# Kernel optimization log

Measured on AMD Instinct MI355X. Metric: run time of the kernel, lower is better.

## Reference

```python
import jax, jax.numpy as jnp
import numpy as np

# decoded layout constants
NN, NO, SD = 16, 8, 4          # num_neighbors, num_obstacles, state_dim_per_agent
B = 131072                      # batch rows
H1, E, HP, AD = 64, 16, 64, 2   # phi hidden, embed, psi hidden, action dim
D_ROBOT, D_OBST = 0.3, 0.3
B_GAMMA, B_EXPH = 0.05, 1.0
PHI_MIN, PHI_MAX = -2.0, 2.0
A_MAX = 2.0


def setup_inputs() -> dict:
    key = jax.random.key(0)
    kx, kw = jax.random.split(key)
    # x: [count | goal(SD) | NN neighbor rel-states (SD each) | NO obstacle rel-pos (2 each)]
    x = jax.random.normal(kx, (B, 1 + SD + SD * NN + 2 * NO), dtype=jnp.float32) * 2.0
    x = x.at[:, 0].set(float(NN))
    names = [("Wp1n", (SD, H1)), ("bp1n", (H1,)), ("Wp2n", (H1, E)), ("bp2n", (E,)),
             ("Wr1n", (E, H1)), ("br1n", (H1,)), ("Wr2n", (H1, E)), ("br2n", (E,)),
             ("Wp1o", (2, H1)), ("bp1o", (H1,)), ("Wp2o", (H1, E)), ("bp2o", (E,)),
             ("Wr1o", (E, H1)), ("br1o", (H1,)), ("Wr2o", (H1, E)), ("br2o", (E,)),
             ("Wpsi1", (2 * E + SD, HP)), ("bpsi1", (HP,)), ("Wpsi2", (HP, AD)), ("bpsi2", (AD,))]
    ks = jax.random.split(kw, len(names))
    inp = {"x": x}
    for (n, sh), k in zip(names, ks):
        s = 1.0 / np.sqrt(sh[0])  # torch Linear default init scale
        inp[n] = jax.random.uniform(k, sh, jnp.float32, -s, s)
    return inp


def _mlp2(h, W1, b1, W2, b2):
    # Feedforward: activation between layers, linear output
    return jax.nn.relu(h @ W1 + b1) @ W2 + b2


def _deepset(el, Wp1, bp1, Wp2, bp2, Wr1, br1, Wr2, br2):
    # el: [B, n, d] -> phi each element, sum over set, rho
    phi = _mlp2(el, Wp1, bp1, Wp2, bp2)          # [B, n, E]
    return _mlp2(phi.sum(axis=1), Wr1, br1, Wr2, br2)  # [B, E]


def _barrier_sum(P, D):
    # P: [B, n, 2]; APF barrier gamma * P / (|P| * (|P|-D)^exph), summed over n
    nrm = jnp.linalg.norm(P, axis=-1, keepdims=True)   # [B, n, 1]
    H = nrm - D
    return (B_GAMMA * P / (nrm * H ** B_EXPH)).sum(axis=1)  # [B, 2]


def reference(x, Wp1n, bp1n, Wp2n, bp2n, Wr1n, br1n, Wr2n, br2n,
              Wp1o, bp1o, Wp2o, bp2o, Wr1o, br1o, Wr2o, br2o,
              Wpsi1, bpsi1, Wpsi2, bpsi2):
    nb = x.shape[0]
    g = x[:, 1:1 + SD]                                        # goal
    nbr = x[:, 1 + SD:1 + SD + SD * NN].reshape(nb, NN, SD)   # neighbor rel-states
    obs = x[:, 1 + SD + SD * NN:].reshape(nb, NO, 2)          # obstacle rel-pos

    rho_n = _deepset(nbr, Wp1n, bp1n, Wp2n, bp2n, Wr1n, br1n, Wr2n, br2n)
    rho_o = _deepset(obs, Wp1o, bp1o, Wp2o, bp2o, Wr1o, br1o, Wr2o, br2o)

    h = jnp.concatenate([rho_n, rho_o, g], axis=1)            # [B, 2E+SD]
    emp = _mlp2(h, Wpsi1, bpsi1, Wpsi2, bpsi2)                # psi network
    emp = (jnp.tanh(emp) + 1.0) / 2.0 * (PHI_MAX - PHI_MIN) + PHI_MIN  # scale_empty

    bar = _barrier_sum(-nbr[:, :, :2], D_ROBOT) + _barrier_sum(-obs, D_OBST)

    action = emp + bar
    # scale(): divide rows whose inf-norm exceeds a_max
    inv_alpha = jnp.maximum(jnp.max(jnp.abs(action), axis=1, keepdims=True) / A_MAX, 1.0)
    return action / inv_alpha
```

## Files before the change

### kernel.cpp

```cpp
#include <hip/hip_runtime.h>
#include <math.h>


typedef __attribute__((ext_vector_type(8))) _Float16 f16x8;
typedef __attribute__((ext_vector_type(2))) __fp16 fp16x2;
typedef __attribute__((ext_vector_type(4))) float f32x4;

#define XW 85

#define FR_S1N  0
#define FR_S1O  4
#define FR_G2N  8
#define FR_G2O  10
#define FR_RNA  12
#define FR_RNB  16
#define FR_ROA  18
#define FR_ROB  22
#define FR_PSI1 24
#define FR_PSI2 32
#define N_FRAGS 34

#define BIG_STR 144
#define PHI_STR 80
#define CAT_STR 144
#define L_BIG  0
#define L_PHI  2304
#define L_CAT  3584
#define L_OUT  5888
#define L_BAR  6016
#define L_OBA  6144
#define GRP_LDS 6688
#define NBA_STR 136
#define OBA_STR 68

#define H16_ONE 0x00003C00u

__device__ __forceinline__ float fast_rcp(float x)  { return __builtin_amdgcn_rcpf(x); }
__device__ __forceinline__ float fast_sqrt(float x) { return __builtin_amdgcn_sqrtf(x); }

__device__ __forceinline__ float two_tanh(float a) {
    float ax = fabsf(a);
    float e = __expf(2.0f * ax);
    float t = 1.0f - 2.0f * fast_rcp(e + 1.0f);
    return copysignf(2.0f * t, a);
}

__device__ __forceinline__ void lds_order() {
    __asm__ __volatile__("" ::: "memory");
}

__device__ __forceinline__ unsigned pk2(float a, float b) {
    union { fp16x2 h; unsigned u; } t;
    t.h = __builtin_amdgcn_cvt_pkrtz(a, b);
    return t.u;
}
__device__ __forceinline__ f16x8 lds_af(const char* area, int stride, int off, int lane) {
    int mm = lane & 15, qq = lane >> 4;
    return *(const f16x8*)(area + mm * stride + off + qq * 16);
}
__device__ __forceinline__ f16x8 load_bh(const _Float16* wsf, int frag, int lane) {
    return ((const f16x8*)(wsf + (size_t)frag * 512))[lane];
}
__device__ __forceinline__ f32x4 cinit(float b) {
    f32x4 c; c[0] = b; c[1] = b; c[2] = b; c[3] = b; return c;
}
__device__ __forceinline__ f32x4 mfma1(f16x8 a, f16x8 b, f32x4 c) {
    return __builtin_amdgcn_mfma_f32_16x16x32_f16(a, b, c, 0, 0, 0);
}

__global__ void bn_prep(const float* __restrict__ Wp1n, const float* __restrict__ Wp2n,
                        const float* __restrict__ Wr1n, const float* __restrict__ Wr2n,
                        const float* __restrict__ Wp1o, const float* __restrict__ Wp2o,
                        const float* __restrict__ Wr1o, const float* __restrict__ Wr2o,
                        const float* __restrict__ Wpsi1, const float* __restrict__ Wpsi2,
                        const float* __restrict__ bp1n, const float* __restrict__ bp1o,
                        const float* __restrict__ br1n, const float* __restrict__ br1o,
                        const float* __restrict__ bpsi1,
                        _Float16* __restrict__ wsf)
{
    int f = blockIdx.x;
    int lane = threadIdx.x;
    const float* W; const float* bias = nullptr;
    int K, N, kk = 0, nt = 0, rel, kbias = -1;
    float wscale = 1.0f;
    if (f < 4)        { W = Wp1n;  K = 4;  N = 64; nt = f;      bias = bp1n;  kbias = 4; }
    else if (f < 8)   { W = Wp1o;  K = 2;  N = 64; nt = f - 4;  bias = bp1o;  kbias = 2; }
    else if (f < 10)  { W = Wp2n;  K = 64; N = 16; kk = f - 8;  wscale = 0.5f; }
    else if (f < 12)  { W = Wp2o;  K = 64; N = 16; kk = f - 10; wscale = 0.5f; }
    else if (f < 16)  { W = Wr1n;  K = 16; N = 64; nt = f - 12; bias = br1n;  kbias = 16; }
    else if (f < 18)  { W = Wr2n;  K = 64; N = 16; kk = f - 16; }
    else if (f < 22)  { W = Wr1o;  K = 16; N = 64; nt = f - 18; bias = br1o;  kbias = 16; }
    else if (f < 24)  { W = Wr2o;  K = 64; N = 16; kk = f - 22; }
    else if (f < 32)  { rel = f - 24; W = Wpsi1; K = 36; N = 64; kk = rel >> 2; nt = rel & 3;
                        bias = bpsi1; kbias = 36; }
    else              { W = Wpsi2; K = 64; N = 2;  kk = f - 32; }

    int q = lane >> 4, c = lane & 15;
    _Float16* dst = wsf + (size_t)f * 512 + lane * 8;
    for (int j = 0; j < 8; ++j) {
        int k = kk * 32 + q * 8 + j;
        int n = nt * 16 + c;
        float v = 0.f;
        if (n < N) {
            if (k < K) v = W[k * N + n] * wscale;
            else if (k == kbias) v = bias[n];
        }
        dst[j] = (_Float16)v;
    }
}

__global__ __launch_bounds__(256, 5) void bn_main(
    const float* __restrict__ x, const _Float16* __restrict__ wsf,
    const float* __restrict__ bp2n, const float* __restrict__ br2n,
    const float* __restrict__ bp2o, const float* __restrict__ br2o,
    const float* __restrict__ bpsi2,
    float* __restrict__ out, int nb)
{
    __shared__ char smem[4 * GRP_LDS];
    const int lane = threadIdx.x & 63;
    const int wid  = threadIdx.x >> 6;
    const int group = blockIdx.x * 4 + wid;
    const int row0 = group * 16;

    char* Gl   = smem + wid * GRP_LDS;
    char* BIG  = Gl + L_BIG;
    char* PHI  = Gl + L_PHI;
    char* CAT  = Gl + L_CAT;
    char* OUTA = Gl + L_OUT;
    char* BAR  = Gl + L_BAR;
    char* OBA  = Gl + L_OBA;
    char* NBA  = BIG;

    const int m = lane & 15, q = lane >> 4, c = m;
    const float* xg   = x + (size_t)row0 * XW;
    const float* xrow = xg + (size_t)m * XW;

    const f32x4 ZC = cinit(0.f);

    {
        int ln5 = lane >> 5;
        int pr  = lane & 31;
        int mm0 = pr >> 1, fp = pr & 1;
        char* db = NBA + mm0 * NBA_STR + fp * 4;
        const float* s0 = xg + (size_t)ln5 * XW + 5 + pr * 2;
        #pragma unroll
        for (int t = 0; t < 8; ++t) {
            const float* s = s0 + (size_t)(2 * t) * XW;
            *(unsigned*)(db + (2 * t + ln5) * 8) = pk2(s[0], s[1]);
        }
    }
    {
        int r8 = lane >> 3;
        int oo = lane & 7;
        char* db = OBA + oo * OBA_STR;
        const float* s0 = xg + (size_t)r8 * XW + 69 + oo * 2;
        #pragma unroll
        for (int t = 0; t < 2; ++t) {
            const float* s = s0 + (size_t)(8 * t) * XW;
            *(unsigned*)(db + (8 * t + r8) * 4) = pk2(s[0], s[1]);
        }
    }

    {
        unsigned zv = ((lane & 7) == 0) ? H16_ONE : 0u;
        for (int i = lane; i < 128; i += 64) {
            int r = i >> 3, d = i & 7;
            *(unsigned*)(PHI + r * PHI_STR + 32 + d * 4) = zv;
        }
    }
    {
        unsigned zc = ((lane & 15) == 2) ? H16_ONE : 0u;
        for (int i = lane; i < 256; i += 64) {
            int r = i >> 4, d = i & 15;
            *(unsigned*)(CAT + r * CAT_STR + 64 + d * 4) = zc;
        }
    }
    if (lane < 16) {
        const float* xr = x + (size_t)(row0 + lane) * XW;
        uint2 gv;
        gv.x = pk2(xr[1], xr[2]);
        gv.y = pk2(xr[3], xr[4]);
        *(uint2*)(CAT + lane * CAT_STR + 64) = gv;
    }

    {
        float bx = 0.f, by = 0.f;
        #pragma unroll
        for (int i = 0; i < 4; ++i) {
            int n = 4 * q + i;
            float px = -xrow[5 + 4 * n], py = -xrow[6 + 4 * n];
            float nrm = fast_sqrt(px * px + py * py);
            float coef = 0.05f * fast_rcp(nrm * (nrm - 0.3f));
            bx = fmaf(coef, px, bx);
            by = fmaf(coef, py, by);
        }
        #pragma unroll
        for (int i = 0; i < 2; ++i) {
            int o = 2 * q + i;
            float px = -xrow[69 + 2 * o], py = -xrow[70 + 2 * o];
            float nrm = fast_sqrt(px * px + py * py);
            float coef = 0.05f * fast_rcp(nrm * (nrm - 0.3f));
            bx = fmaf(coef, px, bx);
            by = fmaf(coef, py, by);
        }
        bx += __shfl_xor(bx, 16); by += __shfl_xor(by, 16);
        bx += __shfl_xor(bx, 32); by += __shfl_xor(by, 32);
        if (q == 0) { float2 bb; bb.x = bx; bb.y = by; *(float2*)(BAR + m * 8) = bb; }
    }
    lds_order();

    {
        f16x8 Bs1n[4];
        #pragma unroll
        for (int nt = 0; nt < 4; ++nt) Bs1n[nt] = load_bh(wsf, FR_S1N + nt, lane);

        const int m8 = m * 8;
        f32x4 accS[4], accA[4];
        #pragma unroll
        for (int nt = 0; nt < 4; ++nt) { accS[nt] = cinit(0.f); accA[nt] = cinit(0.f); }
        union { f16x8 v; unsigned u[4]; uint2 h[2]; } A;
        A.u[2] = H16_ONE; A.u[3] = 0;
        #pragma unroll
        for (int mm = 0; mm < 16; ++mm) {
            A.h[0] = *(const uint2*)(NBA + mm * NBA_STR + m8);
            #pragma unroll
            for (int nt = 0; nt < 4; ++nt) {
                accS[nt] = mfma1(A.v, Bs1n[nt], accS[nt]);
                f32x4 cc = mfma1(A.v, Bs1n[nt], ZC);
                #pragma unroll
                for (int reg = 0; reg < 4; ++reg)
                    accA[nt][reg] += fabsf(cc[reg]);
            }
        }
        lds_order();
        #pragma unroll
        for (int nt = 0; nt < 4; ++nt)
            #pragma unroll
            for (int reg = 0; reg < 4; ++reg)
                *(_Float16*)(BIG + (q * 4 + reg) * BIG_STR + (nt * 16 + c) * 2)
                    = (_Float16)(accS[nt][reg] + accA[nt][reg]);
    }
    lds_order();

    {
        float b_g2n = 16.f * bp2n[c];
        f16x8 Bg2n0 = load_bh(wsf, FR_G2N + 0, lane);
        f16x8 Bg2n1 = load_bh(wsf, FR_G2N + 1, lane);
        f16x8 A0 = lds_af(BIG, BIG_STR, 0, lane);
        f16x8 A1 = lds_af(BIG, BIG_STR, 64, lane);
        f32x4 ca = mfma1(A0, Bg2n0, cinit(b_g2n));
        f32x4 cb = mfma1(A1, Bg2n1, ZC);
        #pragma unroll
        for (int reg = 0; reg < 4; ++reg)
            *(_Float16*)(PHI + (q * 4 + reg) * PHI_STR + c * 2) = (_Float16)(ca[reg] + cb[reg]);
    }
    lds_order();

    {
        f16x8 Brna[4];
        #pragma unroll
        for (int nt = 0; nt < 4; ++nt) Brna[nt] = load_bh(wsf, FR_RNA + nt, lane);
        f16x8 A = lds_af(PHI, PHI_STR, 0, lane);
        #pragma unroll
        for (int nt = 0; nt < 4; ++nt) {
            f32x4 cc = mfma1(A, Brna[nt], ZC);
            #pragma unroll
            for (int reg = 0; reg < 4; ++reg)
                *(_Float16*)(BIG + (q * 4 + reg) * BIG_STR + (nt * 16 + c) * 2) = (_Float16)fmaxf(cc[reg], 0.f);
        }
    }
    lds_order();

    {
        float b_rnb = br2n[c];
        f16x8 Brnb0 = load_bh(wsf, FR_RNB + 0, lane);
        f16x8 Brnb1 = load_bh(wsf, FR_RNB + 1, lane);
        f16x8 A0 = lds_af(BIG, BIG_STR, 0, lane);
        f16x8 A1 = lds_af(BIG, BIG_STR, 64, lane);
        f32x4 ca = mfma1(A0, Brnb0, cinit(b_rnb));
        f32x4 cb = mfma1(A1, Brnb1, ZC);
        #pragma unroll
        for (int reg = 0; reg < 4; ++reg)
            *(_Float16*)(CAT + (q * 4 + reg) * CAT_STR + c * 2) = (_Float16)(ca[reg] + cb[reg]);
    }
    lds_order();

    {
        f16x8 Bs1o[4];
        #pragma unroll
        for (int nt = 0; nt < 4; ++nt) Bs1o[nt] = load_bh(wsf, FR_S1O + nt, lane);

        const int m4 = m * 4;
        f32x4 accS[4], accA[4];
        #pragma unroll
        for (int nt = 0; nt < 4; ++nt) { accS[nt] = cinit(0.f); accA[nt] = cinit(0.f); }
        union { f16x8 v; unsigned u[4]; } A;
        A.u[1] = H16_ONE; A.u[2] = 0; A.u[3] = 0;
        #pragma unroll
        for (int oo = 0; oo < 8; ++oo) {
            A.u[0] = *(const unsigned*)(OBA + oo * OBA_STR + m4);
            #pragma unroll
            for (int nt = 0; nt < 4; ++nt) {
                accS[nt] = mfma1(A.v, Bs1o[nt], accS[nt]);
                f32x4 cc = mfma1(A.v, Bs1o[nt], ZC);
                #pragma unroll
                for (int reg = 0; reg < 4; ++reg)
                    accA[nt][reg] += fabsf(cc[reg]);
            }
        }
        lds_order();
        #pragma unroll
        for (int nt = 0; nt < 4; ++nt)
            #pragma unroll
            for (int reg = 0; reg < 4; ++reg)
                *(_Float16*)(BIG + (q * 4 + reg) * BIG_STR + (nt * 16 + c) * 2)
                    = (_Float16)(accS[nt][reg] + accA[nt][reg]);
    }
    lds_order();

    {
        float b_g2o = 8.f * bp2o[c];
        f16x8 Bg2o0 = load_bh(wsf, FR_G2O + 0, lane);
        f16x8 Bg2o1 = load_bh(wsf, FR_G2O + 1, lane);
        f16x8 A0 = lds_af(BIG, BIG_STR, 0, lane);
        f16x8 A1 = lds_af(BIG, BIG_STR, 64, lane);
        f32x4 ca = mfma1(A0, Bg2o0, cinit(b_g2o));
        f32x4 cb = mfma1(A1, Bg2o1, ZC);
        #pragma unroll
        for (int reg = 0; reg < 4; ++reg)
            *(_Float16*)(PHI + (q * 4 + reg) * PHI_STR + c * 2) = (_Float16)(ca[reg] + cb[reg]);
    }
    lds_order();

    {
        f16x8 Broa[4];
        #pragma unroll
        for (int nt = 0; nt < 4; ++nt) Broa[nt] = load_bh(wsf, FR_ROA + nt, lane);
        f16x8 A = lds_af(PHI, PHI_STR, 0, lane);
        #pragma unroll
        for (int nt = 0; nt < 4; ++nt) {
            f32x4 cc = mfma1(A, Broa[nt], ZC);
            #pragma unroll
            for (int reg = 0; reg < 4; ++reg)
                *(_Float16*)(BIG + (q * 4 + reg) * BIG_STR + (nt * 16 + c) * 2) = (_Float16)fmaxf(cc[reg], 0.f);
        }
    }
    lds_order();

    {
        float b_rob = br2o[c];
        f16x8 Brob0 = load_bh(wsf, FR_ROB + 0, lane);
        f16x8 Brob1 = load_bh(wsf, FR_ROB + 1, lane);
        f16x8 A0 = lds_af(BIG, BIG_STR, 0, lane);
        f16x8 A1 = lds_af(BIG, BIG_STR, 64, lane);
        f32x4 ca = mfma1(A0, Brob0, cinit(b_rob));
        f32x4 cb = mfma1(A1, Brob1, ZC);
        #pragma unroll
        for (int reg = 0; reg < 4; ++reg)
            *(_Float16*)(CAT + (q * 4 + reg) * CAT_STR + (16 + c) * 2) = (_Float16)(ca[reg] + cb[reg]);
    }
    lds_order();

    {
        f16x8 Bp1a[4], Bp1b[4];
        #pragma unroll
        for (int nt = 0; nt < 4; ++nt) Bp1a[nt] = load_bh(wsf, FR_PSI1 + nt, lane);
        #pragma unroll
        for (int nt = 0; nt < 4; ++nt) Bp1b[nt] = load_bh(wsf, FR_PSI1 + 4 + nt, lane);
        f16x8 A0 = lds_af(CAT, CAT_STR, 0, lane);
        f16x8 A1 = lds_af(CAT, CAT_STR, 64, lane);
        #pragma unroll
        for (int nt = 0; nt < 4; ++nt) {
            f32x4 ca = mfma1(A0, Bp1a[nt], ZC);
            f32x4 cb = mfma1(A1, Bp1b[nt], ZC);
            #pragma unroll
            for (int reg = 0; reg < 4; ++reg)
                *(_Float16*)(BIG + (q * 4 + reg) * BIG_STR + (nt * 16 + c) * 2) = (_Float16)fmaxf(ca[reg] + cb[reg], 0.f);
        }
    }
    lds_order();

    {
        float b_p2 = (c < 2) ? bpsi2[c] : 0.f;
        f16x8 Bp20 = load_bh(wsf, FR_PSI2 + 0, lane);
        f16x8 Bp21 = load_bh(wsf, FR_PSI2 + 1, lane);
        f16x8 A0 = lds_af(BIG, BIG_STR, 0, lane);
        f16x8 A1 = lds_af(BIG, BIG_STR, 64, lane);
        f32x4 ca = mfma1(A0, Bp20, cinit(b_p2));
        f32x4 cb = mfma1(A1, Bp21, ZC);
        if (c < 2) {
            #pragma unroll
            for (int reg = 0; reg < 4; ++reg)
                *(float*)(OUTA + (q * 4 + reg) * 8 + c * 4) = ca[reg] + cb[reg];
        }
    }
    lds_order();

    if (lane < 16) {
        float2 a  = *(const float2*)(OUTA + lane * 8);
        float2 bb = *(const float2*)(BAR + lane * 8);
        float a0 = two_tanh(a.x) + bb.x;
        float a1 = two_tanh(a.y) + bb.y;
        float amax = fmaxf(fabsf(a0), fabsf(a1));
        float inv_alpha = fmaxf(amax * 0.5f, 1.0f);
        float rr = fast_rcp(inv_alpha);
        float2 o; o.x = a0 * rr; o.y = a1 * rr;
        *(float2*)(out + (size_t)(row0 + lane) * 2) = o;
    }
}

extern "C" void kernel_launch(void* const* d_in, const int* in_sizes, int n_in,
                              void* d_out, int out_size, void* d_ws, size_t ws_size,
                              hipStream_t stream) {
    const float* x     = (const float*)d_in[0];
    const float* Wp1n  = (const float*)d_in[1];
    const float* bp1n  = (const float*)d_in[2];
    const float* Wp2n  = (const float*)d_in[3];
    const float* bp2n  = (const float*)d_in[4];
    const float* Wr1n  = (const float*)d_in[5];
    const float* br1n  = (const float*)d_in[6];
    const float* Wr2n  = (const float*)d_in[7];
    const float* br2n  = (const float*)d_in[8];
    const float* Wp1o  = (const float*)d_in[9];
    const float* bp1o  = (const float*)d_in[10];
    const float* Wp2o  = (const float*)d_in[11];
    const float* bp2o  = (const float*)d_in[12];
    const float* Wr1o  = (const float*)d_in[13];
    const float* br1o  = (const float*)d_in[14];
    const float* Wr2o  = (const float*)d_in[15];
    const float* br2o  = (const float*)d_in[16];
    const float* Wpsi1 = (const float*)d_in[17];
    const float* bpsi1 = (const float*)d_in[18];
    const float* Wpsi2 = (const float*)d_in[19];
    const float* bpsi2 = (const float*)d_in[20];
    float* out = (float*)d_out;

    int nb = in_sizes[0] / XW;
    _Float16* wsf = (_Float16*)d_ws;

    bn_prep<<<N_FRAGS, 64, 0, stream>>>(Wp1n, Wp2n, Wr1n, Wr2n,
                                        Wp1o, Wp2o, Wr1o, Wr2o,
                                        Wpsi1, Wpsi2,
                                        bp1n, bp1o, br1n, br1o, bpsi1,
                                        wsf);

    int groups = (nb + 15) / 16;
    int blocks = (groups + 3) / 4;
    bn_main<<<blocks, 256, 0, stream>>>(x, wsf,
                                        bp2n, br2n, bp2o, br2o, bpsi2,
                                        out, nb);
}
```

Baseline: 137.4 us.

## Fold adjacent linear layers into precomputed combined weight matrices

Precomputes fused weight products (Wp2·Wr1 for each deepset, Wr2·Wpsi1 slices, and combined biases) in the prep kernel, so the main kernel skips the 16-wide embedding and rho output layers. The per-tile MLP chain drops from roughly nine MFMA stages to four, with fewer LDS round trips and barriers. Goal features are packed directly into an MFMA A-fragment instead of a staging buffer, and LDS per group shrinks. Folded weights have 64x64 shape, so MFMA count per remaining stage grows, and fp16 rounding of the products may shift accuracy slightly.

```diff
diff --git a/kernel.cpp b/kernel.cpp
--- a/kernel.cpp
+++ b/kernel.cpp
@@ -10,26 +10,21 @@
 
 #define FR_S1N  0
 #define FR_S1O  4
-#define FR_G2N  8
-#define FR_G2O  10
-#define FR_RNA  12
-#define FR_RNB  16
-#define FR_ROA  18
-#define FR_ROB  22
-#define FR_PSI1 24
-#define FR_PSI2 32
-#define N_FRAGS 34
+#define FR_FN   8
+#define FR_FO   16
+#define FR_ZN   24
+#define FR_ZO   32
+#define FR_WG   40
+#define FR_PSI2 44
+#define N_FRAGS 46
 
 #define BIG_STR 144
-#define PHI_STR 80
-#define CAT_STR 144
 #define L_BIG  0
-#define L_PHI  2304
-#define L_CAT  3584
-#define L_OUT  5888
-#define L_BAR  6016
-#define L_OBA  6144
-#define GRP_LDS 6688
+#define L_BIG2 2304
+#define L_OUT  4608
+#define L_BAR  4736
+#define L_OBA  4864
+#define GRP_LDS 5440
 #define NBA_STR 136
 #define OBA_STR 68
 
@@ -74,45 +69,101 @@
                         const float* __restrict__ Wr1o, const float* __restrict__ Wr2o,
                         const float* __restrict__ Wpsi1, const float* __restrict__ Wpsi2,
                         const float* __restrict__ bp1n, const float* __restrict__ bp1o,
+                        const float* __restrict__ bp2n, const float* __restrict__ bp2o,
                         const float* __restrict__ br1n, const float* __restrict__ br1o,
+                        const float* __restrict__ br2n, const float* __restrict__ br2o,
                         const float* __restrict__ bpsi1,
                         _Float16* __restrict__ wsf)
 {
     int f = blockIdx.x;
     int lane = threadIdx.x;
-    const float* W; const float* bias = nullptr;
-    int K, N, kk = 0, nt = 0, rel, kbias = -1;
-    float wscale = 1.0f;
-    if (f < 4)        { W = Wp1n;  K = 4;  N = 64; nt = f;      bias = bp1n;  kbias = 4; }
-    else if (f < 8)   { W = Wp1o;  K = 2;  N = 64; nt = f - 4;  bias = bp1o;  kbias = 2; }
-    else if (f < 10)  { W = Wp2n;  K = 64; N = 16; kk = f - 8;  wscale = 0.5f; }
-    else if (f < 12)  { W = Wp2o;  K = 64; N = 16; kk = f - 10; wscale = 0.5f; }
-    else if (f < 16)  { W = Wr1n;  K = 16; N = 64; nt = f - 12; bias = br1n;  kbias = 16; }
-    else if (f < 18)  { W = Wr2n;  K = 64; N = 16; kk = f - 16; }
-    else if (f < 22)  { W = Wr1o;  K = 16; N = 64; nt = f - 18; bias = br1o;  kbias = 16; }
-    else if (f < 24)  { W = Wr2o;  K = 64; N = 16; kk = f - 22; }
-    else if (f < 32)  { rel = f - 24; W = Wpsi1; K = 36; N = 64; kk = rel >> 2; nt = rel & 3;
-                        bias = bpsi1; kbias = 36; }
-    else              { W = Wpsi2; K = 64; N = 2;  kk = f - 32; }
-
     int q = lane >> 4, c = lane & 15;
-    _Float16* dst = wsf + (size_t)f * 512 + lane * 8;
-    for (int j = 0; j < 8; ++j) {
-        int k = kk * 32 + q * 8 + j;
-        int n = nt * 16 + c;
-        float v = 0.f;
-        if (n < N) {
-            if (k < K) v = W[k * N + n] * wscale;
-            else if (k == kbias) v = bias[n];
-        }
-        dst[j] = (_Float16)v;
+
+    if (f >= N_FRAGS) {
+        float* dst = (float*)(wsf + (size_t)N_FRAGS * 512) + (f - N_FRAGS) * 64;
+        if (lane < 64) {
+            float s = 0.f;
+            if (f == N_FRAGS) {
+                for (int e = 0; e < 16; ++e) s = fmaf(bp2n[e], Wr1n[e * 64 + lane], s);
+                dst[lane] = 16.f * s + br1n[lane];
+            } else {
+                for (int e = 0; e < 16; ++e) s = fmaf(bp2o[e], Wr1o[e * 64 + lane], s);
+                dst[lane] = 8.f * s + br1o[lane];
+            }
+        }
+        return;
+    }
+
+    _Float16* dstf = wsf + (size_t)f * 512 + lane * 8;
+
+    if (f < 8) {
+        const float* W   = (f < 4) ? Wp1n : Wp1o;
+        const float* bia = (f < 4) ? bp1n : bp1o;
+        int K  = (f < 4) ? 4 : 2;
+        int nt = f & 3;
+        for (int j = 0; j < 8; ++j) {
+            int k = q * 8 + j;
+            int n = nt * 16 + c;
+            float v = 0.f;
+            if (k < K) v = W[k * 64 + n];
+            else if (k == K) v = bia[n];
+            dstf[j] = (_Float16)v;
+        }
+    } else if (f < 24) {
+        int rel = (f - 8) & 7;
+        bool isN = f < 16;
+        const float* Wa = isN ? Wp2n : Wp2o;
+        const float* Wb = isN ? Wr1n : Wr1o;
+        int kk = rel >> 2, nt = rel & 3;
+        for (int j = 0; j < 8; ++j) {
+            int k = kk * 32 + q * 8 + j;
+            int n = nt * 16 + c;
+            float s = 0.f;
+            for (int e = 0; e < 16; ++e) s = fmaf(Wa[k * 16 + e], Wb[e * 64 + n], s);
+            dstf[j] = (_Float16)(0.5f * s);
+        }
+    } else if (f < 40) {
+        int rel = (f - 24) & 7;
+        bool isN = f < 32;
+        const float* Wa = isN ? Wr2n : Wr2o;
+        int roff = isN ? 0 : 16;
+        int kk = rel >> 2, nt = rel & 3;
+        for (int j = 0; j < 8; ++j) {
+            int k = kk * 32 + q * 8 + j;
+            int n = nt * 16 + c;
+            float s = 0.f;
+            for (int e = 0; e < 16; ++e) s = fmaf(Wa[k * 16 + e], Wpsi1[(roff + e) * 64 + n], s);
+            dstf[j] = (_Float16)s;
+        }
+    } else if (f < 44) {
+        int nt = f - 40;
+        for (int j = 0; j < 8; ++j) {
+            int k = q * 8 + j;
+            int n = nt * 16 + c;
+            float v = 0.f;
+            if (k < 4) v = Wpsi1[(32 + k) * 64 + n];
+            else if (k == 4) {
+                float s = bpsi1[n];
+                for (int e = 0; e < 16; ++e) {
+                    s = fmaf(br2n[e], Wpsi1[e * 64 + n], s);
+                    s = fmaf(br2o[e], Wpsi1[(16 + e) * 64 + n], s);
+                }
+                v = s;
+            }
+            dstf[j] = (_Float16)v;
+        }
+    } else {
+        int kk = f - 44;
+        for (int j = 0; j < 8; ++j) {
+            int k = kk * 32 + q * 8 + j;
+            float v = (c < 2) ? Wpsi2[k * 2 + c] : 0.f;
+            dstf[j] = (_Float16)v;
+        }
     }
 }
 
 __global__ __launch_bounds__(256, 5) void bn_main(
     const float* __restrict__ x, const _Float16* __restrict__ wsf,
-    const float* __restrict__ bp2n, const float* __restrict__ br2n,
-    const float* __restrict__ bp2o, const float* __restrict__ br2o,
     const float* __restrict__ bpsi2,
     float* __restrict__ out, int nb)
 {
@@ -124,8 +175,7 @@
 
     char* Gl   = smem + wid * GRP_LDS;
     char* BIG  = Gl + L_BIG;
-    char* PHI  = Gl + L_PHI;
-    char* CAT  = Gl + L_CAT;
+    char* BIG2 = Gl + L_BIG2;
     char* OUTA = Gl + L_OUT;
     char* BAR  = Gl + L_BAR;
     char* OBA  = Gl + L_OBA;
@@ -134,6 +184,9 @@
     const int m = lane & 15, q = lane >> 4, c = m;
     const float* xg   = x + (size_t)row0 * XW;
     const float* xrow = xg + (size_t)m * XW;
+
+    const float* BFN = (const float*)(wsf + (size_t)N_FRAGS * 512);
+    const float* BFO = BFN + 64;
 
     const f32x4 ZC = cinit(0.f);
 
@@ -159,28 +212,6 @@
             const float* s = s0 + (size_t)(8 * t) * XW;
             *(unsigned*)(db + (8 * t + r8) * 4) = pk2(s[0], s[1]);
         }
-    }
-
-    {
-        unsigned zv = ((lane & 7) == 0) ? H16_ONE : 0u;
-        for (int i = lane; i < 128; i += 64) {
-            int r = i >> 3, d = i & 7;
-            *(unsigned*)(PHI + r * PHI_STR + 32 + d * 4) = zv;
-        }
-    }
-    {
-        unsigned zc = ((lane & 15) == 2) ? H16_ONE : 0u;
-        for (int i = lane; i < 256; i += 64) {
-            int r = i >> 4, d = i & 15;
-            *(unsigned*)(CAT + r * CAT_STR + 64 + d * 4) = zc;
-        }
-    }
-    if (lane < 16) {
-        const float* xr = x + (size_t)(row0 + lane) * XW;
-        uint2 gv;
-        gv.x = pk2(xr[1], xr[2]);
-        gv.y = pk2(xr[3], xr[4]);
-        *(uint2*)(CAT + lane * CAT_STR + 64) = gv;
     }
 
     {
@@ -243,49 +274,6 @@
     lds_order();
 
     {
-        float b_g2n = 16.f * bp2n[c];
-        f16x8 Bg2n0 = load_bh(wsf, FR_G2N + 0, lane);
-        f16x8 Bg2n1 = load_bh(wsf, FR_G2N + 1, lane);
-        f16x8 A0 = lds_af(BIG, BIG_STR, 0, lane);
-        f16x8 A1 = lds_af(BIG, BIG_STR, 64, lane);
-        f32x4 ca = mfma1(A0, Bg2n0, cinit(b_g2n));
-        f32x4 cb = mfma1(A1, Bg2n1, ZC);
-        #pragma unroll
-        for (int reg = 0; reg < 4; ++reg)
-            *(_Float16*)(PHI + (q * 4 + reg) * PHI_STR + c * 2) = (_Float16)(ca[reg] + cb[reg]);
-    }
-    lds_order();
-
-    {
-        f16x8 Brna[4];
-        #pragma unroll
-        for (int nt = 0; nt < 4; ++nt) Brna[nt] = load_bh(wsf, FR_RNA + nt, lane);
-        f16x8 A = lds_af(PHI, PHI_STR, 0, lane);
-        #pragma unroll
-        for (int nt = 0; nt < 4; ++nt) {
-            f32x4 cc = mfma1(A, Brna[nt], ZC);
-            #pragma unroll
-            for (int reg = 0; reg < 4; ++reg)
-                *(_Float16*)(BIG + (q * 4 + reg) * BIG_STR + (nt * 16 + c) * 2) = (_Float16)fmaxf(cc[reg], 0.f);
-        }
-    }
-    lds_order();
-
-    {
-        float b_rnb = br2n[c];
-        f16x8 Brnb0 = load_bh(wsf, FR_RNB + 0, lane);
-        f16x8 Brnb1 = load_bh(wsf, FR_RNB + 1, lane);
-        f16x8 A0 = lds_af(BIG, BIG_STR, 0, lane);
-        f16x8 A1 = lds_af(BIG, BIG_STR, 64, lane);
-        f32x4 ca = mfma1(A0, Brnb0, cinit(b_rnb));
-        f32x4 cb = mfma1(A1, Brnb1, ZC);
-        #pragma unroll
-        for (int reg = 0; reg < 4; ++reg)
-            *(_Float16*)(CAT + (q * 4 + reg) * CAT_STR + c * 2) = (_Float16)(ca[reg] + cb[reg]);
-    }
-    lds_order();
-
-    {
         f16x8 Bs1o[4];
         #pragma unroll
         for (int nt = 0; nt < 4; ++nt) Bs1o[nt] = load_bh(wsf, FR_S1O + nt, lane);
@@ -308,74 +296,79 @@
                     accA[nt][reg] += fabsf(cc[reg]);
             }
         }
-        lds_order();
         #pragma unroll
         for (int nt = 0; nt < 4; ++nt)
             #pragma unroll
             for (int reg = 0; reg < 4; ++reg)
-                *(_Float16*)(BIG + (q * 4 + reg) * BIG_STR + (nt * 16 + c) * 2)
+                *(_Float16*)(BIG2 + (q * 4 + reg) * BIG_STR + (nt * 16 + c) * 2)
                     = (_Float16)(accS[nt][reg] + accA[nt][reg]);
     }
     lds_order();
 
     {
-        float b_g2o = 8.f * bp2o[c];
-        f16x8 Bg2o0 = load_bh(wsf, FR_G2O + 0, lane);
-        f16x8 Bg2o1 = load_bh(wsf, FR_G2O + 1, lane);
         f16x8 A0 = lds_af(BIG, BIG_STR, 0, lane);
         f16x8 A1 = lds_af(BIG, BIG_STR, 64, lane);
-        f32x4 ca = mfma1(A0, Bg2o0, cinit(b_g2o));
-        f32x4 cb = mfma1(A1, Bg2o1, ZC);
-        #pragma unroll
-        for (int reg = 0; reg < 4; ++reg)
-            *(_Float16*)(PHI + (q * 4 + reg) * PHI_STR + c * 2) = (_Float16)(ca[reg] + cb[reg]);
-    }
-    lds_order();
-
-    {
-        f16x8 Broa[4];
-        #pragma unroll
-        for (int nt = 0; nt < 4; ++nt) Broa[nt] = load_bh(wsf, FR_ROA + nt, lane);
-        f16x8 A = lds_af(PHI, PHI_STR, 0, lane);
+        lds_order();
         #pragma unroll
         for (int nt = 0; nt < 4; ++nt) {
-            f32x4 cc = mfma1(A, Broa[nt], ZC);
-            #pragma unroll
-            for (int reg = 0; reg < 4; ++reg)
-                *(_Float16*)(BIG + (q * 4 + reg) * BIG_STR + (nt * 16 + c) * 2) = (_Float16)fmaxf(cc[reg], 0.f);
-        }
-    }
-    lds_order();
-
-    {
-        float b_rob = br2o[c];
-        f16x8 Brob0 = load_bh(wsf, FR_ROB + 0, lane);
-        f16x8 Brob1 = load_bh(wsf, FR_ROB + 1, lane);
-        f16x8 A0 = lds_af(BIG, BIG_STR, 0, lane);
-        f16x8 A1 = lds_af(BIG, BIG_STR, 64, lane);
-        f32x4 ca = mfma1(A0, Brob0, cinit(b_rob));
-        f32x4 cb = mfma1(A1, Brob1, ZC);
-        #pragma unroll
-        for (int reg = 0; reg < 4; ++reg)
-            *(_Float16*)(CAT + (q * 4 + reg) * CAT_STR + (16 + c) * 2) = (_Float16)(ca[reg] + cb[reg]);
-    }
-    lds_order();
-
-    {
-        f16x8 Bp1a[4], Bp1b[4];
-        #pragma unroll
-        for (int nt = 0; nt < 4; ++nt) Bp1a[nt] = load_bh(wsf, FR_PSI1 + nt, lane);
-        #pragma unroll
-        for (int nt = 0; nt < 4; ++nt) Bp1b[nt] = load_bh(wsf, FR_PSI1 + 4 + nt, lane);
-        f16x8 A0 = lds_af(CAT, CAT_STR, 0, lane);
-        f16x8 A1 = lds_af(CAT, CAT_STR, 64, lane);
+            f16x8 B0 = load_bh(wsf, FR_FN + nt, lane);
+            f16x8 B1 = load_bh(wsf, FR_FN + 4 + nt, lane);
+            f32x4 cc = mfma1(A0, B0, cinit(BFN[nt * 16 + c]));
+            cc = mfma1(A1, B1, cc);
+            #pragma unroll
+            for (int reg = 0; reg < 4; ++reg)
+                *(_Float16*)(BIG + (q * 4 + reg) * BIG_STR + (nt * 16 + c) * 2)
+                    = (_Float16)fmaxf(cc[reg], 0.f);
+        }
+    }
+    lds_order();
+
+    {
+        f16x8 A0 = lds_af(BIG2, BIG_STR, 0, lane);
+        f16x8 A1 = lds_af(BIG2, BIG_STR, 64, lane);
+        lds_order();
         #pragma unroll
         for (int nt = 0; nt < 4; ++nt) {
-            f32x4 ca = mfma1(A0, Bp1a[nt], ZC);
-            f32x4 cb = mfma1(A1, Bp1b[nt], ZC);
-            #pragma unroll
-            for (int reg = 0; reg < 4; ++reg)
-                *(_Float16*)(BIG + (q * 4 + reg) * BIG_STR + (nt * 16 + c) * 2) = (_Float16)fmaxf(ca[reg] + cb[reg], 0.f);
+            f16x8 B0 = load_bh(wsf, FR_FO + nt, lane);
+            f16x8 B1 = load_bh(wsf, FR_FO + 4 + nt, lane);
+            f32x4 cc = mfma1(A0, B0, cinit(BFO[nt * 16 + c]));
+            cc = mfma1(A1, B1, cc);
+            #pragma unroll
+            for (int reg = 0; reg < 4; ++reg)
+                *(_Float16*)(BIG2 + (q * 4 + reg) * BIG_STR + (nt * 16 + c) * 2)
+                    = (_Float16)fmaxf(cc[reg], 0.f);
+        }
+    }
+    lds_order();
+
+    {
+        union { f16x8 v; unsigned u[4]; } gA;
+        gA.u[0] = pk2(xrow[1], xrow[2]);
+        gA.u[1] = pk2(xrow[3], xrow[4]);
+        gA.u[2] = H16_ONE;
+        gA.u[3] = 0;
+
+        f16x8 An0 = lds_af(BIG,  BIG_STR, 0, lane);
+        f16x8 An1 = lds_af(BIG,  BIG_STR, 64, lane);
+        f16x8 Ao0 = lds_af(BIG2, BIG_STR, 0, lane);
+        f16x8 Ao1 = lds_af(BIG2, BIG_STR, 64, lane);
+        lds_order();
+        #pragma unroll
+        for (int nt = 0; nt < 4; ++nt) {
+            f16x8 Bg  = load_bh(wsf, FR_WG + nt, lane);
+            f16x8 Bn0 = load_bh(wsf, FR_ZN + nt, lane);
+            f16x8 Bn1 = load_bh(wsf, FR_ZN + 4 + nt, lane);
+            f16x8 Bo0 = load_bh(wsf, FR_ZO + nt, lane);
+            f16x8 Bo1 = load_bh(wsf, FR_ZO + 4 + nt, lane);
+            f32x4 cc = mfma1(gA.v, Bg, ZC);
+            cc = mfma1(An0, Bn0, cc);
+            cc = mfma1(An1, Bn1, cc);
+            cc = mfma1(Ao0, Bo0, cc);
+            cc = mfma1(Ao1, Bo1, cc);
+            #pragma unroll
+            for (int reg = 0; reg < 4; ++reg)
+                *(_Float16*)(BIG + (q * 4 + reg) * BIG_STR + (nt * 16 + c) * 2)
+                    = (_Float16)fmaxf(cc[reg], 0.f);
         }
     }
     lds_order();
@@ -438,15 +431,14 @@
     int nb = in_sizes[0] / XW;
     _Float16* wsf = (_Float16*)d_ws;
 
-    bn_prep<<<N_FRAGS, 64, 0, stream>>>(Wp1n, Wp2n, Wr1n, Wr2n,
-                                        Wp1o, Wp2o, Wr1o, Wr2o,
-                                        Wpsi1, Wpsi2,
-                                        bp1n, bp1o, br1n, br1o, bpsi1,
-                                        wsf);
+    bn_prep<<<N_FRAGS + 2, 64, 0, stream>>>(Wp1n, Wp2n, Wr1n, Wr2n,
+                                            Wp1o, Wp2o, Wr1o, Wr2o,
+                                            Wpsi1, Wpsi2,
+                                            bp1n, bp1o, bp2n, bp2o,
+                                            br1n, br1o, br2n, br2o,
+                                            bpsi1, wsf);
 
     int groups = (nb + 15) / 16;
     int blocks = (groups + 3) / 4;
-    bn_main<<<blocks, 256, 0, stream>>>(x, wsf,
-                                        bp2n, br2n, bp2o, br2o, bpsi2,
-                                        out, nb);
-}
+    bn_main<<<blocks, 256, 0, stream>>>(x, wsf, bpsi2, out, nb);
+}
```

Result: slower. 140.3 us (+2.1%).
